# Kernel optimization log

Measured on AMD Instinct MI355X. Metric: run time of the kernel, lower is better.

## Reference

```python
import jax, jax.numpy as jnp
import numpy as np

N = 256        # num_nodes
F = 256        # feature_dim
B = 32         # batch
DEG = 32       # out-degree per node -> E = N*DEG edges


def setup_inputs() -> dict:
    key = jax.random.key(0)
    k1, k2, k3, k4 = jax.random.split(key, 4)
    node_features = jax.random.normal(k1, (B, N, F), dtype=jnp.float32)
    # xavier_uniform for [N, N, F] tensor: fan_in = N*F, fan_out = N*F per torch default flattening
    limit = float(np.sqrt(6.0 / (N * F + N * F)))
    W = jax.random.uniform(k2, (N, N, F), dtype=jnp.float32, minval=-limit, maxval=limit)
    phase = jax.random.uniform(k3, (N, N), dtype=jnp.float32, minval=0.0, maxval=2.0 * np.pi)
    # topology: each node i has DEG outgoing connections (paths[i])
    src = jnp.repeat(jnp.arange(N, dtype=jnp.int64), DEG)              # [E]
    dst = jax.random.randint(k4, (N * DEG,), 0, N, dtype=jnp.int64)    # [E]
    return {"node_features": node_features, "W": W, "phase": phase, "src": src, "dst": dst}


def reference(node_features, W, phase, src, dst):
    # real(exp(i*phase)) == cos(phase); per-edge effective weight [E, F]
    eff_w = W[src, dst, :] * jnp.cos(phase[src, dst])[:, None]
    # gather source node features and scale: [B, E, F]
    signal = node_features[:, src, :] * eff_w[None, :, :]
    # scatter-add into destination nodes
    propagated = jnp.zeros_like(node_features).at[:, dst, :].add(signal)
    # normalization by out-degree of each node index (matches original indexing)
    n = node_features.shape[1]
    counts = jnp.zeros((n,), dtype=node_features.dtype).at[src].add(1.0)
    norm = jnp.maximum(counts, 1.0)
    return propagated / norm[None, :, None]
```

## Files before the change

kernel.cpp:

```cpp
#include <hip/hip_runtime.h>
#include <math.h>

#define NN 256
#define FF 256
#define BB 32
#define EE 8192


#define FGROUPS 8
#define CAP 96

__global__ __launch_bounds__(256, 8) void fused_propagate_kernel(
    const float4* __restrict__ nf4,
    const float4* __restrict__ W4,
    const float*  __restrict__ phase,
    const int*    __restrict__ dst,
    float4*       __restrict__ out4)
{
    const int fg   = blockIdx.x & (FGROUPS - 1);
    const int d    = blockIdx.x >> 3;
    const int tid  = threadIdx.x;
    const int lane = tid & 63;
    const int wv   = tid >> 6;

    __shared__ int  scnt[NN];
    __shared__ int2 lsa[CAP];
    __shared__ int  wtot[4];

    const int4* dstq = (const int4*)dst;
    int c[8];
    #pragma unroll
    for (int i = 0; i < 8; i++) {
        const int4 v = dstq[tid + 256 * i];
        c[i] = (v.x == d) + (v.y == d) + (v.z == d) + (v.w == d);
    }
    #pragma unroll
    for (int off = 1; off < 8; off <<= 1) {
        #pragma unroll
        for (int i = 0; i < 8; i++) c[i] += __shfl_xor(c[i], off, 64);
    }
    if ((tid & 7) == 0) {
        const int g = tid >> 3;
        #pragma unroll
        for (int i = 0; i < 8; i++) scnt[g + 32 * i] = c[i];
    }
    __syncthreads();

    const int cnt = scnt[tid];
    const int ind = (cnt > 0) ? 1 : 0;

    const unsigned long long mask  = __ballot(ind);
    const int                below = __popcll(mask & ((1ULL << lane) - 1ULL));
    if (lane == 0) wtot[wv] = __popcll(mask);
    __syncthreads();

    int wbase = 0;
    #pragma unroll
    for (int w = 0; w < 4; w++) wbase += (w < wv) ? wtot[w] : 0;
    const int total = wtot[0] + wtot[1] + wtot[2] + wtot[3];

    if (ind) {
        const float a = (float)cnt * cosf(phase[tid * NN + d]) * 0.03125f;
        lsa[wbase + below] = make_int2(tid, __float_as_int(a));
    }
    const int n4 = (total + 3) & ~3;
    if (tid < n4 - total) lsa[total + tid] = make_int2(0, 0);
    __syncthreads();

    const int f4  = fg * (FF / 4 / FGROUPS) + (tid & 7);
    const int b   = tid >> 3;
    const int nfb = b * (NN * FF / 4) + f4;
    const int wdb = d * (FF / 4) + f4;

    float4 acc = {0.f, 0.f, 0.f, 0.f};
    for (int k = 0; k < n4; k += 4) {
        const int2 e0 = lsa[k + 0], e1 = lsa[k + 1], e2 = lsa[k + 2], e3 = lsa[k + 3];
        const int   s0 = e0.x, s1 = e1.x, s2 = e2.x, s3 = e3.x;
        const float a0 = __int_as_float(e0.y), a1 = __int_as_float(e1.y);
        const float a2 = __int_as_float(e2.y), a3 = __int_as_float(e3.y);

        float4 w0 = W4[s0 * (NN * FF / 4) + wdb];
        float4 w1 = W4[s1 * (NN * FF / 4) + wdb];
        float4 w2 = W4[s2 * (NN * FF / 4) + wdb];
        float4 w3 = W4[s3 * (NN * FF / 4) + wdb];
        const float4 x0 = nf4[nfb + s0 * (FF / 4)];
        const float4 x1 = nf4[nfb + s1 * (FF / 4)];
        const float4 x2 = nf4[nfb + s2 * (FF / 4)];
        const float4 x3 = nf4[nfb + s3 * (FF / 4)];

        w0.x *= a0; w0.y *= a0; w0.z *= a0; w0.w *= a0;
        w1.x *= a1; w1.y *= a1; w1.z *= a1; w1.w *= a1;
        w2.x *= a2; w2.y *= a2; w2.z *= a2; w2.w *= a2;
        w3.x *= a3; w3.y *= a3; w3.z *= a3; w3.w *= a3;

        acc.x = fmaf(x0.x, w0.x, acc.x); acc.y = fmaf(x0.y, w0.y, acc.y);
        acc.z = fmaf(x0.z, w0.z, acc.z); acc.w = fmaf(x0.w, w0.w, acc.w);
        acc.x = fmaf(x1.x, w1.x, acc.x); acc.y = fmaf(x1.y, w1.y, acc.y);
        acc.z = fmaf(x1.z, w1.z, acc.z); acc.w = fmaf(x1.w, w1.w, acc.w);
        acc.x = fmaf(x2.x, w2.x, acc.x); acc.y = fmaf(x2.y, w2.y, acc.y);
        acc.z = fmaf(x2.z, w2.z, acc.z); acc.w = fmaf(x2.w, w2.w, acc.w);
        acc.x = fmaf(x3.x, w3.x, acc.x); acc.y = fmaf(x3.y, w3.y, acc.y);
        acc.z = fmaf(x3.z, w3.z, acc.z); acc.w = fmaf(x3.w, w3.w, acc.w);
    }

    out4[b * (NN * FF / 4) + d * (FF / 4) + f4] = acc;
}

extern "C" void kernel_launch(void* const* d_in, const int* in_sizes, int n_in,
                              void* d_out, int out_size, void* d_ws, size_t ws_size,
                              hipStream_t stream) {
    const float* nf    = (const float*)d_in[0];
    const float* W     = (const float*)d_in[1];
    const float* phase = (const float*)d_in[2];
    const int*   dst   = (const int*)d_in[4];
    float*       out   = (float*)d_out;

    fused_propagate_kernel<<<NN * FGROUPS, 256, 0, stream>>>(
        (const float4*)nf, (const float4*)W, phase, dst, (float4*)out);
}
```

Before: 124.1 us.

## Stage scaled W rows in shared memory and software-pipeline feature gathers

Before the main loop, each block now loads the scaled W slice for every contributing source once into shared memory. Previously each of the 32 batch-row threads re-read the same W values from global memory and scaled them itself. The accumulation loop then prefetches the next four node-feature gathers while doing FMAs on the current ones. In exchange it uses about 12KB more LDS per block, adds a sync, and lowers the launch-bounds occupancy hint from 8 to 4 blocks.

```diff
diff --git a/kernel.cpp b/kernel.cpp
--- a/kernel.cpp
+++ b/kernel.cpp
@@ -10,7 +10,7 @@
 #define FGROUPS 8
 #define CAP 96
 
-__global__ __launch_bounds__(256, 8) void fused_propagate_kernel(
+__global__ __launch_bounds__(256, 4) void fused_propagate_kernel(
     const float4* __restrict__ nf4,
     const float4* __restrict__ W4,
     const float*  __restrict__ phase,
@@ -23,9 +23,10 @@
     const int lane = tid & 63;
     const int wv   = tid >> 6;
 
-    __shared__ int  scnt[NN];
-    __shared__ int2 lsa[CAP];
-    __shared__ int  wtot[4];
+    __shared__ int    scnt[NN];
+    __shared__ int2   lsa[CAP];
+    __shared__ int    wtot[4];
+    __shared__ float4 aw4[CAP * 8];
 
     const int4* dstq = (const int4*)dst;
     int c[8];
@@ -67,43 +68,72 @@
     if (tid < n4 - total) lsa[total + tid] = make_int2(0, 0);
     __syncthreads();
 
-    const int f4  = fg * (FF / 4 / FGROUPS) + (tid & 7);
+    const int wrow = d * (FF / 4) + fg * 8;
+    for (int slot = tid; slot < n4 * 8; slot += 256) {
+        const int  e = slot >> 3, f = slot & 7;
+        const int2 sa = lsa[e];
+        const float a = __int_as_float(sa.y);
+        float4 w = W4[sa.x * (NN * FF / 4) + wrow + f];
+        w.x *= a; w.y *= a; w.z *= a; w.w *= a;
+        aw4[slot] = w;
+    }
+    __syncthreads();
+
+    const int myf = tid & 7;
     const int b   = tid >> 3;
-    const int nfb = b * (NN * FF / 4) + f4;
-    const int wdb = d * (FF / 4) + f4;
+    const int nfb = b * (NN * FF / 4) + fg * 8 + myf;
 
     float4 acc = {0.f, 0.f, 0.f, 0.f};
-    for (int k = 0; k < n4; k += 4) {
-        const int2 e0 = lsa[k + 0], e1 = lsa[k + 1], e2 = lsa[k + 2], e3 = lsa[k + 3];
-        const int   s0 = e0.x, s1 = e1.x, s2 = e2.x, s3 = e3.x;
-        const float a0 = __int_as_float(e0.y), a1 = __int_as_float(e1.y);
-        const float a2 = __int_as_float(e2.y), a3 = __int_as_float(e3.y);
 
-        float4 w0 = W4[s0 * (NN * FF / 4) + wdb];
-        float4 w1 = W4[s1 * (NN * FF / 4) + wdb];
-        float4 w2 = W4[s2 * (NN * FF / 4) + wdb];
-        float4 w3 = W4[s3 * (NN * FF / 4) + wdb];
-        const float4 x0 = nf4[nfb + s0 * (FF / 4)];
-        const float4 x1 = nf4[nfb + s1 * (FF / 4)];
-        const float4 x2 = nf4[nfb + s2 * (FF / 4)];
-        const float4 x3 = nf4[nfb + s3 * (FF / 4)];
+    if (n4 > 0) {
+        int s0 = lsa[0].x, s1 = lsa[1].x, s2 = lsa[2].x, s3 = lsa[3].x;
+        float4 x0 = nf4[nfb + s0 * (FF / 4)];
+        float4 x1 = nf4[nfb + s1 * (FF / 4)];
+        float4 x2 = nf4[nfb + s2 * (FF / 4)];
+        float4 x3 = nf4[nfb + s3 * (FF / 4)];
 
-        w0.x *= a0; w0.y *= a0; w0.z *= a0; w0.w *= a0;
-        w1.x *= a1; w1.y *= a1; w1.z *= a1; w1.w *= a1;
-        w2.x *= a2; w2.y *= a2; w2.z *= a2; w2.w *= a2;
-        w3.x *= a3; w3.y *= a3; w3.z *= a3; w3.w *= a3;
+        for (int k = 4; k < n4; k += 4) {
+            const int t0 = lsa[k + 0].x, t1 = lsa[k + 1].x;
+            const int t2 = lsa[k + 2].x, t3 = lsa[k + 3].x;
+            const float4 y0 = nf4[nfb + t0 * (FF / 4)];
+            const float4 y1 = nf4[nfb + t1 * (FF / 4)];
+            const float4 y2 = nf4[nfb + t2 * (FF / 4)];
+            const float4 y3 = nf4[nfb + t3 * (FF / 4)];
 
-        acc.x = fmaf(x0.x, w0.x, acc.x); acc.y = fmaf(x0.y, w0.y, acc.y);
-        acc.z = fmaf(x0.z, w0.z, acc.z); acc.w = fmaf(x0.w, w0.w, acc.w);
-        acc.x = fmaf(x1.x, w1.x, acc.x); acc.y = fmaf(x1.y, w1.y, acc.y);
-        acc.z = fmaf(x1.z, w1.z, acc.z); acc.w = fmaf(x1.w, w1.w, acc.w);
-        acc.x = fmaf(x2.x, w2.x, acc.x); acc.y = fmaf(x2.y, w2.y, acc.y);
-        acc.z = fmaf(x2.z, w2.z, acc.z); acc.w = fmaf(x2.w, w2.w, acc.w);
-        acc.x = fmaf(x3.x, w3.x, acc.x); acc.y = fmaf(x3.y, w3.y, acc.y);
-        acc.z = fmaf(x3.z, w3.z, acc.z); acc.w = fmaf(x3.w, w3.w, acc.w);
+            {
+                const float4 a0 = aw4[(k - 4) * 8 + myf];
+                const float4 a1 = aw4[(k - 3) * 8 + myf];
+                const float4 a2 = aw4[(k - 2) * 8 + myf];
+                const float4 a3 = aw4[(k - 1) * 8 + myf];
+                acc.x = fmaf(x0.x, a0.x, acc.x); acc.y = fmaf(x0.y, a0.y, acc.y);
+                acc.z = fmaf(x0.z, a0.z, acc.z); acc.w = fmaf(x0.w, a0.w, acc.w);
+                acc.x = fmaf(x1.x, a1.x, acc.x); acc.y = fmaf(x1.y, a1.y, acc.y);
+                acc.z = fmaf(x1.z, a1.z, acc.z); acc.w = fmaf(x1.w, a1.w, acc.w);
+                acc.x = fmaf(x2.x, a2.x, acc.x); acc.y = fmaf(x2.y, a2.y, acc.y);
+                acc.z = fmaf(x2.z, a2.z, acc.z); acc.w = fmaf(x2.w, a2.w, acc.w);
+                acc.x = fmaf(x3.x, a3.x, acc.x); acc.y = fmaf(x3.y, a3.y, acc.y);
+                acc.z = fmaf(x3.z, a3.z, acc.z); acc.w = fmaf(x3.w, a3.w, acc.w);
+            }
+            x0 = y0; x1 = y1; x2 = y2; x3 = y3;
+        }
+
+        {
+            const float4 a0 = aw4[(n4 - 4) * 8 + myf];
+            const float4 a1 = aw4[(n4 - 3) * 8 + myf];
+            const float4 a2 = aw4[(n4 - 2) * 8 + myf];
+            const float4 a3 = aw4[(n4 - 1) * 8 + myf];
+            acc.x = fmaf(x0.x, a0.x, acc.x); acc.y = fmaf(x0.y, a0.y, acc.y);
+            acc.z = fmaf(x0.z, a0.z, acc.z); acc.w = fmaf(x0.w, a0.w, acc.w);
+            acc.x = fmaf(x1.x, a1.x, acc.x); acc.y = fmaf(x1.y, a1.y, acc.y);
+            acc.z = fmaf(x1.z, a1.z, acc.z); acc.w = fmaf(x1.w, a1.w, acc.w);
+            acc.x = fmaf(x2.x, a2.x, acc.x); acc.y = fmaf(x2.y, a2.y, acc.y);
+            acc.z = fmaf(x2.z, a2.z, acc.z); acc.w = fmaf(x2.w, a2.w, acc.w);
+            acc.x = fmaf(x3.x, a3.x, acc.x); acc.y = fmaf(x3.y, a3.y, acc.y);
+            acc.z = fmaf(x3.z, a3.z, acc.z); acc.w = fmaf(x3.w, a3.w, acc.w);
+        }
     }
 
-    out4[b * (NN * FF / 4) + d * (FF / 4) + f4] = acc;
+    out4[b * (NN * FF / 4) + d * (FF / 4) + fg * 8 + myf] = acc;
 }
 
 extern "C" void kernel_launch(void* const* d_in, const int* in_sizes, int n_in,
```

Result: faster. 116.1 us (-6.4%).
